# Optimization experiments

Hardware: AMD Instinct MI355X
Metric: run time of the kernel (lower is better)

## Reference

```python
import jax, jax.numpy as jnp
import numpy as np

NUM_GROUPS = 8
EPS = 1e-5


def setup_inputs() -> dict:
    key = jax.random.key(0)
    ks = jax.random.split(key, 4)
    C = 128
    x = jax.random.normal(ks[0], (4, C, 64, 64), dtype=jnp.float32)
    gn_weight = jnp.ones((C,), dtype=jnp.float32)
    gn_bias = jnp.zeros((C,), dtype=jnp.float32)
    qkv_weight = jax.random.normal(ks[1], (3 * C, C), dtype=jnp.float32) * (C ** -0.5)
    qkv_bias = jnp.zeros((3 * C,), dtype=jnp.float32)
    proj_weight = jax.random.normal(ks[2], (C, C), dtype=jnp.float32) * (C ** -0.5)
    proj_bias = jnp.zeros((C,), dtype=jnp.float32)
    return {
        "x": x,
        "gn_weight": gn_weight,
        "gn_bias": gn_bias,
        "qkv_weight": qkv_weight,
        "qkv_bias": qkv_bias,
        "proj_weight": proj_weight,
        "proj_bias": proj_bias,
    }


def reference(x, gn_weight, gn_bias, qkv_weight, qkv_bias, proj_weight, proj_bias):
    b, c, h, w = x.shape
    scale = c ** (-0.5)

    # GroupNorm(8, c): normalize over (channels_in_group, h, w)
    xg = x.reshape(b, NUM_GROUPS, c // NUM_GROUPS, h, w)
    mean = jnp.mean(xg, axis=(2, 3, 4), keepdims=True)
    var = jnp.var(xg, axis=(2, 3, 4), keepdims=True)
    xn = ((xg - mean) * jax.lax.rsqrt(var + EPS)).reshape(b, c, h, w)
    xn = xn * gn_weight[None, :, None, None] + gn_bias[None, :, None, None]

    # 1x1 conv QKV == channel matmul; flatten spatial to sequence n = h*w
    xn_flat = xn.reshape(b, c, h * w)  # [b, c, n]
    qkv = jnp.einsum('oc,bcn->bno', qkv_weight, xn_flat) + qkv_bias  # [b, n, 3c]
    q, k, v = qkv[..., :c], qkv[..., c:2 * c], qkv[..., 2 * c:]

    # attention: materializes [b, n, n] scores as in original
    attn = jnp.einsum('bnc,bmc->bnm', q, k) * scale
    attn = jax.nn.softmax(attn, axis=-1)
    out = jnp.einsum('bnm,bmc->bnc', attn, v)  # [b, n, c]

    # proj 1x1 conv + residual
    out = jnp.einsum('oc,bnc->bno', proj_weight, out) + proj_bias  # [b, n, c]
    out = out.transpose(0, 2, 1).reshape(b, c, h, w)
    return x + out
```

## Files before the change

kernel.cpp:

```cpp
#include <hip/hip_runtime.h>

#define BATCH 4
#define CCH 128
#define NSP 4096
#define NGRP 8
#define GROUP_ELEMS 65536
#define QSCALE 0.12751744f
#define EPS_GN 1e-5f
#define OPSTRIDE 2097152
#define LPSTRIDE 16384

typedef short s8b __attribute__((ext_vector_type(8)));
typedef float f32x4 __attribute__((ext_vector_type(4)));
typedef float f32x16 __attribute__((ext_vector_type(16)));

static __device__ __forceinline__ short f2bf(float f) {
  union { float f; unsigned u; } v; v.f = f;
  unsigned r = (v.u + 0x7FFFu + ((v.u >> 16) & 1u)) >> 16;
  return (short)r;
}

static __device__ __forceinline__ float bf2f(short s) {
  unsigned u = ((unsigned)(unsigned short)s) << 16;
  float f; __builtin_memcpy(&f, &u, 4); return f;
}

static __device__ __forceinline__ float fexp2(float x) {
#if __has_builtin(__builtin_amdgcn_exp2f)
  return __builtin_amdgcn_exp2f(x);
#else
  return exp2f(x);
#endif
}

static __device__ __forceinline__ unsigned pack2bf(float a, float b) {
  unsigned ua, ub;
  __builtin_memcpy(&ua, &a, 4); __builtin_memcpy(&ub, &b, 4);
  ua += 0x8000u; ub += 0x8000u;
#if __has_builtin(__builtin_amdgcn_perm)
  return __builtin_amdgcn_perm(ub, ua, 0x07060302u);
#else
  return (ua >> 16) | (ub & 0xFFFF0000u);
#endif
}

static __device__ __forceinline__ s8b pack8(float a0, float a1, float a2, float a3,
                                            float a4, float a5, float a6, float a7) {
  union { unsigned u[4]; s8b v; } x;
  x.u[0] = pack2bf(a0, a1); x.u[1] = pack2bf(a2, a3);
  x.u[2] = pack2bf(a4, a5); x.u[3] = pack2bf(a6, a7);
  return x.v;
}

static __device__ __forceinline__ f32x4 mfma16(s8b a, s8b b, f32x4 c) {
  return __builtin_amdgcn_mfma_f32_16x16x32_bf16(a, b, c, 0, 0, 0);
}
static __device__ __forceinline__ f32x16 mfma32(s8b a, s8b b, f32x16 c) {
  return __builtin_amdgcn_mfma_f32_32x32x16_bf16(a, b, c, 0, 0, 0);
}

static __device__ __forceinline__ void async16(const void* g, void* l) {
  __builtin_amdgcn_global_load_lds(
      (const __attribute__((address_space(1))) void*)g,
      (__attribute__((address_space(3))) void*)l, 16, 0, 0);
}

__global__ void gn_stats(const float* __restrict__ x, float* __restrict__ part) {
  int bx = blockIdx.x;
  int ch = bx & 7, bg = bx >> 3;
  const float* base = x + (size_t)bg * GROUP_ELEMS + (size_t)ch * 8192;
  int t = threadIdx.x;
  float s = 0.f, ss = 0.f;
  #pragma unroll
  for (int i = 0; i < 8; ++i) {
    float4 v = *(const float4*)(base + i * 1024 + t * 4);
    s  += v.x + v.y + v.z + v.w;
    ss += v.x * v.x + v.y * v.y + v.z * v.z + v.w * v.w;
  }
  #pragma unroll
  for (int off = 1; off < 64; off <<= 1) {
    s  += __shfl_xor(s, off);
    ss += __shfl_xor(ss, off);
  }
  __shared__ float red[8];
  int w = t >> 6;
  if ((t & 63) == 0) { red[w * 2] = s; red[w * 2 + 1] = ss; }
  __syncthreads();
  if (t == 0) {
    part[bx * 2]     = red[0] + red[2] + red[4] + red[6];
    part[bx * 2 + 1] = red[1] + red[3] + red[5] + red[7];
  }
}

__global__ void gn_apply(const float* __restrict__ x, const float* __restrict__ gw,
                         const float* __restrict__ gb, const float* __restrict__ part,
                         short* __restrict__ xn) {
  int bx = blockIdx.x;
  int ns = bx & 7, g = (bx >> 3) & 7, b = bx >> 6;
  int bg = b * NGRP + g;
  float s = 0.f, ss = 0.f;
  #pragma unroll
  for (int j = 0; j < 8; ++j) {
    s  += part[(bg * 8 + j) * 2];
    ss += part[(bg * 8 + j) * 2 + 1];
  }
  float mean = s * (1.f / GROUP_ELEMS);
  float var  = ss * (1.f / GROUP_ELEMS) - mean * mean;
  float inv  = rsqrtf(var + EPS_GN);
  int t = threadIdx.x;
  int cl = t & 15, n4 = t >> 4;
  int c = g * 16 + cl;
  float ga = gw[c] * inv;
  float be = gb[c] - mean * ga;
  const float* xr = x + (size_t)(b * CCH + c) * NSP;
  short* xo = xn + (size_t)b * NSP * CCH + c;
  #pragma unroll
  for (int i = 0; i < 8; ++i) {
    int n = ns * 512 + i * 64 + n4 * 4;
    float4 v = *(const float4*)(xr + n);
    xo[(size_t)(n + 0) * CCH] = f2bf(v.x * ga + be);
    xo[(size_t)(n + 1) * CCH] = f2bf(v.y * ga + be);
    xo[(size_t)(n + 2) * CCH] = f2bf(v.z * ga + be);
    xo[(size_t)(n + 3) * CCH] = f2bf(v.w * ga + be);
  }
}

__global__ void qkv_gemm(const short* __restrict__ xn, const float* __restrict__ Wqkv,
                         const float* __restrict__ bias, short* __restrict__ q,
                         short* __restrict__ k, short* __restrict__ vt) {
  __shared__ short Xl[128 * 136];
  __shared__ short Wl[64 * 136];
  int bx = blockIdx.x;
  int t = threadIdx.x;
  int lane = t & 63, w = t >> 6, l15 = lane & 15, quad = lane >> 4;
  if (bx < 1024) {
    int ot = bx & 3, nt = (bx >> 2) & 63, b = bx >> 8;
    for (int idx = t; idx < 64 * 16; idx += 256) {
      int row = idx >> 4, c8 = idx & 15;
      *(s8b*)&Xl[row * 136 + c8 * 8] =
          *(const s8b*)(xn + ((size_t)(b * NSP + nt * 64 + row)) * CCH + c8 * 8);
    }
    for (int idx = t; idx < 64 * 16; idx += 256) {
      int row = idx >> 4, c8 = idx & 15;
      const float* src = Wqkv + (size_t)(ot * 64 + row) * CCH + c8 * 8;
      s8b wv;
      #pragma unroll
      for (int j = 0; j < 8; ++j) wv[j] = f2bf(src[j]);
      *(s8b*)&Wl[row * 136 + c8 * 8] = wv;
    }
    __syncthreads();
    s8b a[4];
    #pragma unroll
    for (int kc = 0; kc < 4; ++kc)
      a[kc] = *(const s8b*)&Xl[(w * 16 + l15) * 136 + kc * 32 + quad * 8];
    #pragma unroll
    for (int o4 = 0; o4 < 4; ++o4) {
      f32x4 acc = {0.f, 0.f, 0.f, 0.f};
      #pragma unroll
      for (int kc = 0; kc < 4; ++kc) {
        s8b bw = *(const s8b*)&Wl[(o4 * 16 + l15) * 136 + kc * 32 + quad * 8];
        acc = mfma16(a[kc], bw, acc);
      }
      int obase = ot * 64 + o4 * 16;
      short* dst = (obase < 128) ? q : k;
      float mulf = (obase < 128) ? QSCALE : 1.0f;
      int oc = obase - ((obase < 128) ? 0 : 128) + l15;
      float bs = bias[obase + l15];
      #pragma unroll
      for (int r = 0; r < 4; ++r) {
        int n = nt * 64 + w * 16 + quad * 4 + r;
        dst[((size_t)(b * NSP + n)) * CCH + oc] = f2bf((acc[r] + bs) * mulf);
      }
    }
  } else {
    int vbx = bx - 1024;
    int ot = vbx & 1, nt = (vbx >> 1) & 31, b = vbx >> 6;
    for (int idx = t; idx < 128 * 16; idx += 256) {
      int row = idx >> 4, c8 = idx & 15;
      *(s8b*)&Xl[row * 136 + c8 * 8] =
          *(const s8b*)(xn + ((size_t)(b * NSP + nt * 128 + row)) * CCH + c8 * 8);
    }
    for (int idx = t; idx < 64 * 16; idx += 256) {
      int row = idx >> 4, c8 = idx & 15;
      const float* src = Wqkv + (size_t)(256 + ot * 64 + row) * CCH + c8 * 8;
      s8b wv;
      #pragma unroll
      for (int j = 0; j < 8; ++j) wv[j] = f2bf(src[j]);
      *(s8b*)&Wl[row * 136 + c8 * 8] = wv;
    }
    __syncthreads();
    s8b a[4];
    #pragma unroll
    for (int kc = 0; kc < 4; ++kc)
      a[kc] = *(const s8b*)&Wl[(w * 16 + l15) * 136 + kc * 32 + quad * 8];
    float bs[4];
    #pragma unroll
    for (int r = 0; r < 4; ++r) bs[r] = bias[256 + ot * 64 + w * 16 + quad * 4 + r];
    int ppos = 8 * ((l15 >> 2) & 1) + (l15 & 3) + 4 * (l15 >> 3);
    #pragma unroll
    for (int ntile = 0; ntile < 8; ++ntile) {
      f32x4 acc = {0.f, 0.f, 0.f, 0.f};
      #pragma unroll
      for (int kc = 0; kc < 4; ++kc) {
        s8b bx2 = *(const s8b*)&Xl[(ntile * 16 + l15) * 136 + kc * 32 + quad * 8];
        acc = mfma16(a[kc], bx2, acc);
      }
      int npos = nt * 128 + ntile * 16 + ppos;
      #pragma unroll
      for (int r = 0; r < 4; ++r) {
        int og = ot * 64 + w * 16 + quad * 4 + r;
        vt[((size_t)(b * CCH + og)) * NSP + npos] = f2bf(acc[r] + bs[r]);
      }
    }
  }
}

__global__ __launch_bounds__(256, 2) void flash(const short* __restrict__ q,
                                                const short* __restrict__ k,
                                                const short* __restrict__ vt,
                                                short* __restrict__ Op,
                                                float* __restrict__ Lp) {
  int bx = blockIdx.x;
  int kh = bx & 3, b = (bx >> 2) & 3, qt = bx >> 4;
  __shared__ short Kl[2][64 * 128];
  __shared__ short Vl[2][128 * 64];
  int t = threadIdx.x;
  int lane = t & 63, w = t >> 6;
  int l31 = lane & 31, h = lane >> 5;
  const short* kbase = k + (size_t)b * NSP * CCH;
  const short* vbase = vt + (size_t)b * CCH * NSP;
  int kt0 = kh * 1024;

  int krow_in_chunk = lane >> 4, kgrp = lane & 15;
  int vrow_in_chunk = lane >> 3, vgrp = lane & 7;

  s8b aq[8];
  {
    const short* qp = q + ((size_t)(b * NSP + qt * 128 + w * 32 + l31)) * CCH + h * 8;
    #pragma unroll
    for (int kc = 0; kc < 8; ++kc) aq[kc] = *(const s8b*)(qp + kc * 16);
  }
  f32x16 O[4];
  #pragma unroll
  for (int cg = 0; cg < 4; ++cg)
    #pragma unroll
    for (int r = 0; r < 16; ++r) O[cg][r] = 0.f;
  float lsum = 0.f;

  #define STAGE(buf_, key0_)                                                        \
    {                                                                               \
      const int key0v = (key0_);                                                    \
      _Pragma("unroll") for (int si = 0; si < 4; ++si) {                            \
        int c = w * 4 + si;                                                         \
        int rt = c * 4 + krow_in_chunk;                                             \
        async16(kbase + (size_t)(key0v + rt) * CCH + ((kgrp ^ (rt & 15)) * 8),      \
                &Kl[buf_][c * 512]);                                                \
        int rc = c * 8 + vrow_in_chunk;                                             \
        async16(vbase + (size_t)rc * NSP + key0v + ((vgrp ^ (rc & 7)) * 8),         \
                &Vl[buf_][c * 512]);                                                \
      }                                                                             \
    }

  STAGE(0, kt0)
  __syncthreads();

  for (int i = 0; i < 16; ++i) {
    int buf = i & 1;
    if (i < 15) STAGE(buf ^ 1, kt0 + (i + 1) * 64)

    s8b pb[4];
    #pragma unroll
    for (int tile = 0; tile < 2; ++tile) {
      f32x16 st;
      #pragma unroll
      for (int r = 0; r < 16; ++r) st[r] = 0.f;
      const short* kp = &Kl[buf][(tile * 32 + l31) * 128];
      #pragma unroll
      for (int kc = 0; kc < 8; ++kc) {
        s8b ak = *(const s8b*)&kp[(((kc * 2 + h) ^ (l31 & 15))) * 8];
        st = mfma32(ak, aq[kc], st);
      }
      float pp[16];
      #pragma unroll
      for (int r = 0; r < 16; ++r) pp[r] = fexp2(st[r]);
      lsum += (((pp[0] + pp[1]) + (pp[2] + pp[3])) + ((pp[4] + pp[5]) + (pp[6] + pp[7]))) +
              (((pp[8] + pp[9]) + (pp[10] + pp[11])) + ((pp[12] + pp[13]) + (pp[14] + pp[15])));
      pb[tile * 2 + 0] = pack8(pp[0], pp[1], pp[2], pp[3], pp[4], pp[5], pp[6], pp[7]);
      pb[tile * 2 + 1] = pack8(pp[8], pp[9], pp[10], pp[11], pp[12], pp[13], pp[14], pp[15]);
    }
    #pragma unroll
    for (int cg = 0; cg < 4; ++cg) {
      const short* vp = &Vl[buf][(cg * 32 + l31) * 64];
      #pragma unroll
      for (int kc2 = 0; kc2 < 4; ++kc2) {
        s8b av = *(const s8b*)&vp[(((kc2 * 2 + h) ^ (l31 & 7))) * 8];
        O[cg] = mfma32(av, pb[kc2], O[cg]);
      }
    }
    __syncthreads();
  }

  lsum += __shfl_xor(lsum, 32);

  short* eb = &Kl[0][0] + w * 4096;
  #pragma unroll
  for (int cg = 0; cg < 4; ++cg)
    #pragma unroll
    for (int rp = 0; rp < 8; ++rp) {
      int r = rp * 2;
      int chlo = (r & 3) + 4 * h;
      int chhi = cg * 4 + (r >> 2);
      *(unsigned*)&eb[l31 * 128 + ((chhi ^ (l31 & 7))) * 8 + chlo] =
          pack2bf(O[cg][r], O[cg][r + 1]);
    }
  short* ob = Op + (size_t)kh * OPSTRIDE + ((size_t)(b * NSP + qt * 128)) * CCH;
  float* lp = Lp + kh * LPSTRIDE + b * NSP + qt * 128;
  if (lane < 32) lp[w * 32 + l31] = lsum;
  __syncthreads();
  for (int idx = t; idx < 128 * 16; idx += 256) {
    int row = idx >> 4, c8 = idx & 15;
    int w2 = row >> 5, nl = row & 31;
    *(s8b*)(ob + (size_t)row * CCH + c8 * 8) =
        *(const s8b*)(&Kl[0][0] + w2 * 4096 + nl * 128 + ((c8 ^ (nl & 7))) * 8);
  }
}

__global__ void proj_gemm(const short* __restrict__ Op, const float* __restrict__ Lp,
                          const float* __restrict__ Wp, const float* __restrict__ pbias,
                          const float* __restrict__ x, float* __restrict__ out) {
  int bx = blockIdx.x;
  int nt = bx & 63, b = bx >> 6;
  __shared__ short Wl[128][136];
  int t = threadIdx.x;
  for (int idx = t; idx < 128 * 16; idx += 256) {
    int row = idx >> 4, c8 = idx & 15;
    const float* src = Wp + (size_t)row * CCH + c8 * 8;
    s8b wv;
    #pragma unroll
    for (int j = 0; j < 8; ++j) wv[j] = f2bf(src[j]);
    *(s8b*)&Wl[row][c8 * 8] = wv;
  }
  __syncthreads();
  int lane = t & 63, w = t >> 6, l15 = lane & 15, quad = lane >> 4;
  int row = nt * 64 + w * 16 + l15;
  float lsum = Lp[0 * LPSTRIDE + b * NSP + row] + Lp[1 * LPSTRIDE + b * NSP + row] +
               Lp[2 * LPSTRIDE + b * NSP + row] + Lp[3 * LPSTRIDE + b * NSP + row];
  float linv = 1.f / lsum;
  const short* ap = Op + ((size_t)(b * NSP + row)) * CCH + quad * 8;
  s8b bfr[4];
  #pragma unroll
  for (int kc = 0; kc < 4; ++kc) {
    float acc8[8];
    #pragma unroll
    for (int j = 0; j < 8; ++j) acc8[j] = 0.f;
    #pragma unroll
    for (int s = 0; s < 4; ++s) {
      s8b tv = *(const s8b*)(ap + (size_t)s * OPSTRIDE + kc * 32);
      #pragma unroll
      for (int j = 0; j < 8; ++j) acc8[j] += bf2f(tv[j]);
    }
    #pragma unroll
    for (int j = 0; j < 8; ++j) bfr[kc][j] = f2bf(acc8[j] * linv);
  }
  #pragma unroll
  for (int cg = 0; cg < 8; ++cg) {
    f32x4 acc = {0.f, 0.f, 0.f, 0.f};
    #pragma unroll
    for (int kc = 0; kc < 4; ++kc) {
      s8b aw = *(const s8b*)&Wl[cg * 16 + l15][kc * 32 + quad * 8];
      acc = mfma16(aw, bfr[kc], acc);
    }
    #pragma unroll
    for (int r = 0; r < 4; ++r) {
      int co = cg * 16 + quad * 4 + r;
      int n = nt * 64 + w * 16 + l15;
      size_t off = ((size_t)(b * CCH + co)) * NSP + n;
      out[off] = x[off] + acc[r] + pbias[co];
    }
  }
}

extern "C" void kernel_launch(void* const* d_in, const int* in_sizes, int n_in,
                              void* d_out, int out_size, void* d_ws, size_t ws_size,
                              hipStream_t stream) {
  (void)in_sizes; (void)n_in; (void)out_size; (void)ws_size;
  const float* x    = (const float*)d_in[0];
  const float* gw   = (const float*)d_in[1];
  const float* gb   = (const float*)d_in[2];
  const float* Wqkv = (const float*)d_in[3];
  const float* bqkv = (const float*)d_in[4];
  const float* Wp   = (const float*)d_in[5];
  const float* bp   = (const float*)d_in[6];
  float* out = (float*)d_out;
  char* ws = (char*)d_ws;
  float* part = (float*)ws;
  short* xn    = (short*)(ws + 4096);
  short* q     = (short*)(ws + 4096 + 1ull * 4194304);
  short* k     = (short*)(ws + 4096 + 2ull * 4194304);
  short* vt    = (short*)(ws + 4096 + 3ull * 4194304);
  short* Opart = (short*)(ws + 4096 + 4ull * 4194304);
  float* Lpart = (float*)(ws + 4096 + 8ull * 4194304);

  gn_stats<<<256, 256, 0, stream>>>(x, part);
  gn_apply<<<256, 256, 0, stream>>>(x, gw, gb, part, xn);
  qkv_gemm<<<1280, 256, 0, stream>>>(xn, Wqkv, bqkv, q, k, vt);
  flash<<<512, 256, 0, stream>>>(q, k, vt, Opart, Lpart);
  proj_gemm<<<256, 256, 0, stream>>>(Opart, Lpart, Wp, bp, x, out);
}
```

Measured before the change: 134.5 us.

## Process two query tiles per wave and split keys eight ways in flash

```diff
diff --git a/kernel.cpp b/kernel.cpp
--- a/kernel.cpp
+++ b/kernel.cpp
@@ -221,31 +221,34 @@
                                                 short* __restrict__ Op,
                                                 float* __restrict__ Lp) {
   int bx = blockIdx.x;
-  int kh = bx & 3, b = (bx >> 2) & 3, qt = bx >> 4;
-  __shared__ short Kl[2][64 * 128];
-  __shared__ short Vl[2][128 * 64];
+  int kh = bx & 7, b = (bx >> 3) & 3, qt = bx >> 5;
+  __shared__ short SMEM[32768];
   int t = threadIdx.x;
   int lane = t & 63, w = t >> 6;
   int l31 = lane & 31, h = lane >> 5;
   const short* kbase = k + (size_t)b * NSP * CCH;
   const short* vbase = vt + (size_t)b * CCH * NSP;
-  int kt0 = kh * 1024;
+  int kt0 = kh * 512;
 
   int krow_in_chunk = lane >> 4, kgrp = lane & 15;
   int vrow_in_chunk = lane >> 3, vgrp = lane & 7;
 
-  s8b aq[8];
+  s8b aq0[8], aq1[8];
   {
-    const short* qp = q + ((size_t)(b * NSP + qt * 128 + w * 32 + l31)) * CCH + h * 8;
-    #pragma unroll
-    for (int kc = 0; kc < 8; ++kc) aq[kc] = *(const s8b*)(qp + kc * 16);
-  }
-  f32x16 O[4];
-  #pragma unroll
-  for (int cg = 0; cg < 4; ++cg)
-    #pragma unroll
-    for (int r = 0; r < 16; ++r) O[cg][r] = 0.f;
-  float lsum = 0.f;
+    const short* qp0 = q + ((size_t)(b * NSP + qt * 256 + w * 64 + l31)) * CCH + h * 8;
+    const short* qp1 = qp0 + 32 * CCH;
+    #pragma unroll
+    for (int kc = 0; kc < 8; ++kc) { aq0[kc] = *(const s8b*)(qp0 + kc * 16);
+                                     aq1[kc] = *(const s8b*)(qp1 + kc * 16); }
+  }
+  f32x16 O[2][4];
+  #pragma unroll
+  for (int g = 0; g < 2; ++g)
+    #pragma unroll
+    for (int cg = 0; cg < 4; ++cg)
+      #pragma unroll
+      for (int r = 0; r < 16; ++r) O[g][cg][r] = 0.f;
+  float lsum0 = 0.f, lsum1 = 0.f;
 
   #define STAGE(buf_, key0_)                                                        \
     {                                                                               \
@@ -254,74 +257,89 @@
         int c = w * 4 + si;                                                         \
         int rt = c * 4 + krow_in_chunk;                                             \
         async16(kbase + (size_t)(key0v + rt) * CCH + ((kgrp ^ (rt & 15)) * 8),      \
-                &Kl[buf_][c * 512]);                                                \
+                &SMEM[(buf_)*8192 + c * 512]);                                      \
         int rc = c * 8 + vrow_in_chunk;                                             \
         async16(vbase + (size_t)rc * NSP + key0v + ((vgrp ^ (rc & 7)) * 8),         \
-                &Vl[buf_][c * 512]);                                                \
+                &SMEM[16384 + (buf_)*8192 + c * 512]);                              \
       }                                                                             \
     }
 
   STAGE(0, kt0)
   __syncthreads();
 
-  for (int i = 0; i < 16; ++i) {
+  for (int i = 0; i < 8; ++i) {
     int buf = i & 1;
-    if (i < 15) STAGE(buf ^ 1, kt0 + (i + 1) * 64)
-
-    s8b pb[4];
+    if (i < 7) STAGE(buf ^ 1, kt0 + (i + 1) * 64)
+
     #pragma unroll
     for (int tile = 0; tile < 2; ++tile) {
-      f32x16 st;
-      #pragma unroll
-      for (int r = 0; r < 16; ++r) st[r] = 0.f;
-      const short* kp = &Kl[buf][(tile * 32 + l31) * 128];
+      f32x16 st0, st1;
+      #pragma unroll
+      for (int r = 0; r < 16; ++r) { st0[r] = 0.f; st1[r] = 0.f; }
+      const short* kp = &SMEM[buf * 8192 + (tile * 32 + l31) * 128];
       #pragma unroll
       for (int kc = 0; kc < 8; ++kc) {
         s8b ak = *(const s8b*)&kp[(((kc * 2 + h) ^ (l31 & 15))) * 8];
-        st = mfma32(ak, aq[kc], st);
-      }
-      float pp[16];
-      #pragma unroll
-      for (int r = 0; r < 16; ++r) pp[r] = fexp2(st[r]);
-      lsum += (((pp[0] + pp[1]) + (pp[2] + pp[3])) + ((pp[4] + pp[5]) + (pp[6] + pp[7]))) +
-              (((pp[8] + pp[9]) + (pp[10] + pp[11])) + ((pp[12] + pp[13]) + (pp[14] + pp[15])));
-      pb[tile * 2 + 0] = pack8(pp[0], pp[1], pp[2], pp[3], pp[4], pp[5], pp[6], pp[7]);
-      pb[tile * 2 + 1] = pack8(pp[8], pp[9], pp[10], pp[11], pp[12], pp[13], pp[14], pp[15]);
-    }
-    #pragma unroll
-    for (int cg = 0; cg < 4; ++cg) {
-      const short* vp = &Vl[buf][(cg * 32 + l31) * 64];
-      #pragma unroll
-      for (int kc2 = 0; kc2 < 4; ++kc2) {
-        s8b av = *(const s8b*)&vp[(((kc2 * 2 + h) ^ (l31 & 7))) * 8];
-        O[cg] = mfma32(av, pb[kc2], O[cg]);
+        st0 = mfma32(ak, aq0[kc], st0);
+        st1 = mfma32(ak, aq1[kc], st1);
+      }
+      s8b pb0[2], pb1[2];
+      {
+        float pp[16];
+        #pragma unroll
+        for (int r = 0; r < 16; ++r) pp[r] = fexp2(st0[r]);
+        lsum0 += (((pp[0]+pp[1])+(pp[2]+pp[3]))+((pp[4]+pp[5])+(pp[6]+pp[7]))) +
+                 (((pp[8]+pp[9])+(pp[10]+pp[11]))+((pp[12]+pp[13])+(pp[14]+pp[15])));
+        pb0[0] = pack8(pp[0],pp[1],pp[2],pp[3],pp[4],pp[5],pp[6],pp[7]);
+        pb0[1] = pack8(pp[8],pp[9],pp[10],pp[11],pp[12],pp[13],pp[14],pp[15]);
+        #pragma unroll
+        for (int r = 0; r < 16; ++r) pp[r] = fexp2(st1[r]);
+        lsum1 += (((pp[0]+pp[1])+(pp[2]+pp[3]))+((pp[4]+pp[5])+(pp[6]+pp[7]))) +
+                 (((pp[8]+pp[9])+(pp[10]+pp[11]))+((pp[12]+pp[13])+(pp[14]+pp[15])));
+        pb1[0] = pack8(pp[0],pp[1],pp[2],pp[3],pp[4],pp[5],pp[6],pp[7]);
+        pb1[1] = pack8(pp[8],pp[9],pp[10],pp[11],pp[12],pp[13],pp[14],pp[15]);
+      }
+      #pragma unroll
+      for (int cg = 0; cg < 4; ++cg) {
+        const short* vp = &SMEM[16384 + buf * 8192 + (cg * 32 + l31) * 64];
+        #pragma unroll
+        for (int kk = 0; kk < 2; ++kk) {
+          s8b av = *(const s8b*)&vp[((((tile * 2 + kk) * 2 + h) ^ (l31 & 7))) * 8];
+          O[0][cg] = mfma32(av, pb0[kk], O[0][cg]);
+          O[1][cg] = mfma32(av, pb1[kk], O[1][cg]);
+        }
       }
     }
     __syncthreads();
   }
 
-  lsum += __shfl_xor(lsum, 32);
-
-  short* eb = &Kl[0][0] + w * 4096;
-  #pragma unroll
-  for (int cg = 0; cg < 4; ++cg)
-    #pragma unroll
-    for (int rp = 0; rp < 8; ++rp) {
-      int r = rp * 2;
-      int chlo = (r & 3) + 4 * h;
-      int chhi = cg * 4 + (r >> 2);
-      *(unsigned*)&eb[l31 * 128 + ((chhi ^ (l31 & 7))) * 8 + chlo] =
-          pack2bf(O[cg][r], O[cg][r + 1]);
-    }
-  short* ob = Op + (size_t)kh * OPSTRIDE + ((size_t)(b * NSP + qt * 128)) * CCH;
-  float* lp = Lp + kh * LPSTRIDE + b * NSP + qt * 128;
-  if (lane < 32) lp[w * 32 + l31] = lsum;
+  lsum0 += __shfl_xor(lsum0, 32);
+  lsum1 += __shfl_xor(lsum1, 32);
+
+  #pragma unroll
+  for (int g = 0; g < 2; ++g) {
+    int nl = w * 64 + g * 32 + l31;
+    short* eb = &SMEM[nl * 128];
+    #pragma unroll
+    for (int cg = 0; cg < 4; ++cg)
+      #pragma unroll
+      for (int rq = 0; rq < 4; ++rq) {
+        const f32x16& Ov = O[g][cg];
+        unsigned lo = pack2bf(Ov[rq * 4 + 0], Ov[rq * 4 + 1]);
+        unsigned hi = pack2bf(Ov[rq * 4 + 2], Ov[rq * 4 + 3]);
+        unsigned long long dv = ((unsigned long long)hi << 32) | lo;
+        int chhi = cg * 4 + rq;
+        *(unsigned long long*)&eb[((chhi ^ (nl & 7)) * 8) + 4 * h] = dv;
+      }
+  }
+  short* ob = Op + (size_t)kh * OPSTRIDE + ((size_t)(b * NSP + qt * 256)) * CCH;
+  float* lp = Lp + kh * LPSTRIDE + b * NSP + qt * 256;
+  if (lane < 32) { lp[w * 64 + l31] = lsum0; lp[w * 64 + 32 + l31] = lsum1; }
   __syncthreads();
-  for (int idx = t; idx < 128 * 16; idx += 256) {
+  for (int idx = t; idx < 256 * 16; idx += 256) {
     int row = idx >> 4, c8 = idx & 15;
-    int w2 = row >> 5, nl = row & 31;
     *(s8b*)(ob + (size_t)row * CCH + c8 * 8) =
-        *(const s8b*)(&Kl[0][0] + w2 * 4096 + nl * 128 + ((c8 ^ (nl & 7))) * 8);
+        *(const s8b*)&SMEM[row * 128 + ((c8 ^ (row & 7))) * 8];
   }
 }
 
@@ -343,8 +361,9 @@
   __syncthreads();
   int lane = t & 63, w = t >> 6, l15 = lane & 15, quad = lane >> 4;
   int row = nt * 64 + w * 16 + l15;
-  float lsum = Lp[0 * LPSTRIDE + b * NSP + row] + Lp[1 * LPSTRIDE + b * NSP + row] +
-               Lp[2 * LPSTRIDE + b * NSP + row] + Lp[3 * LPSTRIDE + b * NSP + row];
+  float lsum = 0.f;
+  #pragma unroll
+  for (int s = 0; s < 8; ++s) lsum += Lp[s * LPSTRIDE + b * NSP + row];
   float linv = 1.f / lsum;
   const short* ap = Op + ((size_t)(b * NSP + row)) * CCH + quad * 8;
   s8b bfr[4];
@@ -354,7 +373,7 @@
     #pragma unroll
     for (int j = 0; j < 8; ++j) acc8[j] = 0.f;
     #pragma unroll
-    for (int s = 0; s < 4; ++s) {
+    for (int s = 0; s < 8; ++s) {
       s8b tv = *(const s8b*)(ap + (size_t)s * OPSTRIDE + kc * 32);
       #pragma unroll
       for (int j = 0; j < 8; ++j) acc8[j] += bf2f(tv[j]);
@@ -399,7 +418,7 @@
   short* k     = (short*)(ws + 4096 + 2ull * 4194304);
   short* vt    = (short*)(ws + 4096 + 3ull * 4194304);
   short* Opart = (short*)(ws + 4096 + 4ull * 4194304);
-  float* Lpart = (float*)(ws + 4096 + 8ull * 4194304);
+  float* Lpart = (float*)(ws + 4096 + 12ull * 4194304);
 
   gn_stats<<<256, 256, 0, stream>>>(x, part);
   gn_apply<<<256, 256, 0, stream>>>(x, gw, gb, part, xn);
```

After: 215.3 us. 1.6x slower.

## Enlarge flash blocks to 256 queries and split keys eight ways

Applied to the files above, without the earlier changes.

```diff
diff --git a/kernel.cpp b/kernel.cpp
--- a/kernel.cpp
+++ b/kernel.cpp
@@ -215,28 +215,27 @@
   }
 }
 
-__global__ __launch_bounds__(256, 2) void flash(const short* __restrict__ q,
+__global__ __launch_bounds__(512, 4) void flash(const short* __restrict__ q,
                                                 const short* __restrict__ k,
                                                 const short* __restrict__ vt,
                                                 short* __restrict__ Op,
                                                 float* __restrict__ Lp) {
   int bx = blockIdx.x;
-  int kh = bx & 3, b = (bx >> 2) & 3, qt = bx >> 4;
-  __shared__ short Kl[2][64 * 128];
-  __shared__ short Vl[2][128 * 64];
+  int kh = bx & 7, b = (bx >> 3) & 3, qt = bx >> 5;
+  __shared__ short SMEM[32768];
   int t = threadIdx.x;
   int lane = t & 63, w = t >> 6;
   int l31 = lane & 31, h = lane >> 5;
   const short* kbase = k + (size_t)b * NSP * CCH;
   const short* vbase = vt + (size_t)b * CCH * NSP;
-  int kt0 = kh * 1024;
+  int kt0 = kh * 512;
 
   int krow_in_chunk = lane >> 4, kgrp = lane & 15;
   int vrow_in_chunk = lane >> 3, vgrp = lane & 7;
 
   s8b aq[8];
   {
-    const short* qp = q + ((size_t)(b * NSP + qt * 128 + w * 32 + l31)) * CCH + h * 8;
+    const short* qp = q + ((size_t)(b * NSP + qt * 256 + w * 32 + l31)) * CCH + h * 8;
     #pragma unroll
     for (int kc = 0; kc < 8; ++kc) aq[kc] = *(const s8b*)(qp + kc * 16);
   }
@@ -250,23 +249,23 @@
   #define STAGE(buf_, key0_)                                                        \
     {                                                                               \
       const int key0v = (key0_);                                                    \
-      _Pragma("unroll") for (int si = 0; si < 4; ++si) {                            \
-        int c = w * 4 + si;                                                         \
+      _Pragma("unroll") for (int si = 0; si < 2; ++si) {                            \
+        int c = w * 2 + si;                                                         \
         int rt = c * 4 + krow_in_chunk;                                             \
         async16(kbase + (size_t)(key0v + rt) * CCH + ((kgrp ^ (rt & 15)) * 8),      \
-                &Kl[buf_][c * 512]);                                                \
+                &SMEM[(buf_)*8192 + c * 512]);                                      \
         int rc = c * 8 + vrow_in_chunk;                                             \
         async16(vbase + (size_t)rc * NSP + key0v + ((vgrp ^ (rc & 7)) * 8),         \
-                &Vl[buf_][c * 512]);                                                \
+                &SMEM[16384 + (buf_)*8192 + c * 512]);                              \
       }                                                                             \
     }
 
   STAGE(0, kt0)
   __syncthreads();
 
-  for (int i = 0; i < 16; ++i) {
+  for (int i = 0; i < 8; ++i) {
     int buf = i & 1;
-    if (i < 15) STAGE(buf ^ 1, kt0 + (i + 1) * 64)
+    if (i < 7) STAGE(buf ^ 1, kt0 + (i + 1) * 64)
 
     s8b pb[4];
     #pragma unroll
@@ -274,7 +273,7 @@
       f32x16 st;
       #pragma unroll
       for (int r = 0; r < 16; ++r) st[r] = 0.f;
-      const short* kp = &Kl[buf][(tile * 32 + l31) * 128];
+      const short* kp = &SMEM[buf * 8192 + (tile * 32 + l31) * 128];
       #pragma unroll
       for (int kc = 0; kc < 8; ++kc) {
         s8b ak = *(const s8b*)&kp[(((kc * 2 + h) ^ (l31 & 15))) * 8];
@@ -290,7 +289,7 @@
     }
     #pragma unroll
     for (int cg = 0; cg < 4; ++cg) {
-      const short* vp = &Vl[buf][(cg * 32 + l31) * 64];
+      const short* vp = &SMEM[16384 + buf * 8192 + (cg * 32 + l31) * 64];
       #pragma unroll
       for (int kc2 = 0; kc2 < 4; ++kc2) {
         s8b av = *(const s8b*)&vp[(((kc2 * 2 + h) ^ (l31 & 7))) * 8];
@@ -302,26 +301,29 @@
 
   lsum += __shfl_xor(lsum, 32);
 
-  short* eb = &Kl[0][0] + w * 4096;
-  #pragma unroll
-  for (int cg = 0; cg < 4; ++cg)
-    #pragma unroll
-    for (int rp = 0; rp < 8; ++rp) {
-      int r = rp * 2;
-      int chlo = (r & 3) + 4 * h;
-      int chhi = cg * 4 + (r >> 2);
-      *(unsigned*)&eb[l31 * 128 + ((chhi ^ (l31 & 7))) * 8 + chlo] =
-          pack2bf(O[cg][r], O[cg][r + 1]);
-    }
-  short* ob = Op + (size_t)kh * OPSTRIDE + ((size_t)(b * NSP + qt * 128)) * CCH;
-  float* lp = Lp + kh * LPSTRIDE + b * NSP + qt * 128;
+  {
+    int nl = w * 32 + l31;
+    short* eb = &SMEM[nl * 128];
+    #pragma unroll
+    for (int cg = 0; cg < 4; ++cg)
+      #pragma unroll
+      for (int rq = 0; rq < 4; ++rq) {
+        const f32x16& Ov = O[cg];
+        unsigned lo = pack2bf(Ov[rq * 4 + 0], Ov[rq * 4 + 1]);
+        unsigned hi = pack2bf(Ov[rq * 4 + 2], Ov[rq * 4 + 3]);
+        unsigned long long dv = ((unsigned long long)hi << 32) | lo;
+        int chhi = cg * 4 + rq;
+        *(unsigned long long*)&eb[((chhi ^ (nl & 7)) * 8) + 4 * h] = dv;
+      }
+  }
+  short* ob = Op + (size_t)kh * OPSTRIDE + ((size_t)(b * NSP + qt * 256)) * CCH;
+  float* lp = Lp + kh * LPSTRIDE + b * NSP + qt * 256;
   if (lane < 32) lp[w * 32 + l31] = lsum;
   __syncthreads();
-  for (int idx = t; idx < 128 * 16; idx += 256) {
+  for (int idx = t; idx < 256 * 16; idx += 512) {
     int row = idx >> 4, c8 = idx & 15;
-    int w2 = row >> 5, nl = row & 31;
     *(s8b*)(ob + (size_t)row * CCH + c8 * 8) =
-        *(const s8b*)(&Kl[0][0] + w2 * 4096 + nl * 128 + ((c8 ^ (nl & 7))) * 8);
+        *(const s8b*)&SMEM[row * 128 + ((c8 ^ (row & 7))) * 8];
   }
 }
 
@@ -343,8 +345,9 @@
   __syncthreads();
   int lane = t & 63, w = t >> 6, l15 = lane & 15, quad = lane >> 4;
   int row = nt * 64 + w * 16 + l15;
-  float lsum = Lp[0 * LPSTRIDE + b * NSP + row] + Lp[1 * LPSTRIDE + b * NSP + row] +
-               Lp[2 * LPSTRIDE + b * NSP + row] + Lp[3 * LPSTRIDE + b * NSP + row];
+  float lsum = 0.f;
+  #pragma unroll
+  for (int s = 0; s < 8; ++s) lsum += Lp[s * LPSTRIDE + b * NSP + row];
   float linv = 1.f / lsum;
   const short* ap = Op + ((size_t)(b * NSP + row)) * CCH + quad * 8;
   s8b bfr[4];
@@ -354,7 +357,7 @@
     #pragma unroll
     for (int j = 0; j < 8; ++j) acc8[j] = 0.f;
     #pragma unroll
-    for (int s = 0; s < 4; ++s) {
+    for (int s = 0; s < 8; ++s) {
       s8b tv = *(const s8b*)(ap + (size_t)s * OPSTRIDE + kc * 32);
       #pragma unroll
       for (int j = 0; j < 8; ++j) acc8[j] += bf2f(tv[j]);
@@ -399,11 +402,11 @@
   short* k     = (short*)(ws + 4096 + 2ull * 4194304);
   short* vt    = (short*)(ws + 4096 + 3ull * 4194304);
   short* Opart = (short*)(ws + 4096 + 4ull * 4194304);
-  float* Lpart = (float*)(ws + 4096 + 8ull * 4194304);
+  float* Lpart = (float*)(ws + 4096 + 12ull * 4194304);
 
   gn_stats<<<256, 256, 0, stream>>>(x, part);
   gn_apply<<<256, 256, 0, stream>>>(x, gw, gb, part, xn);
   qkv_gemm<<<1280, 256, 0, stream>>>(xn, Wqkv, bqkv, q, k, vt);
-  flash<<<512, 256, 0, stream>>>(q, k, vt, Opart, Lpart);
+  flash<<<512, 512, 0, stream>>>(q, k, vt, Opart, Lpart);
   proj_gemm<<<256, 256, 0, stream>>>(Opart, Lpart, Wp, bp, x, out);
 }
```

After: 211.6 us. 57.4% more time.
